# Optimization experiments

Hardware: AMD Instinct MI355X
Metric: run time of the kernel (lower is better)

Reference implementation:

```python
import jax, jax.numpy as jnp
import numpy as np

EPS = 1e-6

def _rmsnorm(x, scale):
    # RMSNorm over last axis (TPNorm pre-norm)
    var = jnp.mean(jnp.square(x), axis=-1, keepdims=True)
    return x * jax.lax.rsqrt(var + EPS) * scale


def setup_inputs() -> dict:
    key = jax.random.key(0)
    ks = jax.random.split(key, 6)
    B, S, D, H, Dh = 2, 2048, 1024, 16, 64
    x = jax.random.normal(ks[0], (B, S, D), dtype=jnp.float32)
    norm_scale = jnp.ones((D,), dtype=jnp.float32)
    # lecun_normal-like scaling: std = 1/sqrt(fan_in)
    wq = jax.random.normal(ks[1], (D, H, Dh), dtype=jnp.float32) / np.sqrt(D)
    wk = jax.random.normal(ks[2], (D, H, Dh), dtype=jnp.float32) / np.sqrt(D)
    wv = jax.random.normal(ks[3], (D, H, Dh), dtype=jnp.float32) / np.sqrt(D)
    w_out = jax.random.normal(ks[4], (H, Dh, D), dtype=jnp.float32) / np.sqrt(H * Dh)
    b_out = jnp.zeros((D,), dtype=jnp.float32)
    return {"x": x, "norm_scale": norm_scale, "wq": wq, "wk": wk, "wv": wv,
            "w_out": w_out, "b_out": b_out}


def reference(x, norm_scale, wq, wk, wv, w_out, b_out):
    dtype = x.dtype
    softmax_dtype = jnp.float32
    h = _rmsnorm(x, norm_scale)                                  # [B,S,D]
    q = jnp.einsum('bsd,dhe->bshe', h, wq)                       # [B,S,H,Dh]
    k = jnp.einsum('bsd,dhe->bshe', h, wk)
    v = jnp.einsum('bsd,dhe->bshe', h, wv)
    head_dim = q.shape[-1]
    scale = head_dim ** (-0.5)
    q = (q * scale).astype(softmax_dtype)
    kf = k.astype(softmax_dtype)
    weights = jnp.einsum('bqhd,bkhd->bhqk', q, kf)               # [B,H,S,S] fp32
    weights = jax.nn.softmax(weights, axis=-1).astype(dtype)
    new_vals = jnp.einsum('bhqk,bkhd->bqhd', weights, v).astype(dtype)
    out = jnp.einsum('bqhe,hed->bqd', new_vals, w_out) + b_out   # [B,S,D]
    return out
```

## Files before the change

kernel.cpp:

```cpp
#include <hip/hip_runtime.h>

typedef unsigned short u16;
typedef unsigned int   u32;
typedef __attribute__((ext_vector_type(8))) short bf16x8;
typedef __attribute__((ext_vector_type(4))) float f32x4;

#define SEQ 2048
#define DIM 1024
#define NH  16
#define DH  64
#define NROW 4096

static __device__ __forceinline__ u16 f2bf(float f){
  u32 u; __builtin_memcpy(&u, &f, 4);
  u32 r = (u + 0x7fffu + ((u >> 16) & 1u)) >> 16;
  return (u16)r;
}
static __device__ __forceinline__ u32 pack2bf(float a, float b){
  u32 ua, ub; __builtin_memcpy(&ua, &a, 4); __builtin_memcpy(&ub, &b, 4);
  return ((ua + 0x8000u) >> 16) | ((ub + 0x8000u) & 0xFFFF0000u);
}
static __device__ __forceinline__ u32 cvt_pk_bf16(float a, float b){
  u32 r;
  asm("v_cvt_pk_bf16_f32 %0, %1, %2" : "=v"(r) : "v"(a), "v"(b));
  return r;
}

#define GLD_LDS(gp, lp) \
  __builtin_amdgcn_global_load_lds( \
      (const __attribute__((address_space(1))) void*)(gp), \
      (__attribute__((address_space(3))) void*)(lp), 16, 0, 0)

#define WAIT_VM(N) asm volatile("s_waitcnt vmcnt(" #N ")" ::: "memory")
#define CFENCE()   asm volatile("" ::: "memory")

__global__ __launch_bounds__(256) void k_rmsnorm(const float* __restrict__ x,
                                                 const float* __restrict__ sc,
                                                 u16* __restrict__ h){
  int row = blockIdx.x, t = threadIdx.x;
  float4 v = ((const float4*)(x + (size_t)row * DIM))[t];
  float ss = v.x*v.x + v.y*v.y + v.z*v.z + v.w*v.w;
  #pragma unroll
  for (int d = 32; d; d >>= 1) ss += __shfl_down(ss, d, 64);
  __shared__ float red[4];
  if ((t & 63) == 0) red[t >> 6] = ss;
  __syncthreads();
  float tot = red[0] + red[1] + red[2] + red[3];
  float rms = rsqrtf(tot * (1.0f / DIM) + 1e-6f);
  float4 s4 = ((const float4*)sc)[t];
  u16 ov[4];
  ov[0] = f2bf(v.x * rms * s4.x);
  ov[1] = f2bf(v.y * rms * s4.y);
  ov[2] = f2bf(v.z * rms * s4.z);
  ov[3] = f2bf(v.w * rms * s4.w);
  ((uint2*)(h + (size_t)row * DIM))[t] = *(uint2*)ov;
}

__global__ __launch_bounds__(256) void k_wtrans(const float* __restrict__ in0,
                                                const float* __restrict__ in1,
                                                const float* __restrict__ in2,
                                                u16* __restrict__ outT){
  __shared__ u16 tile[64][68];
  int t = threadIdx.x;
  int c0 = blockIdx.x * 64;
  int r0 = blockIdx.y * 64;
  int z = blockIdx.z;
  const float* in = (z == 0) ? in0 : ((z == 1) ? in1 : in2);
  u16* out = outT + (size_t)z * (1u << 20);
  #pragma unroll
  for (int i = 0; i < 4; i++){
    int idx = t + 256 * i;
    int r = idx >> 4, c4 = (idx & 15) * 4;
    float4 v = *(const float4*)&in[(size_t)(r0 + r) * 1024 + c0 + c4];
    u16 pk[4] = {f2bf(v.x), f2bf(v.y), f2bf(v.z), f2bf(v.w)};
    *(uint2*)&tile[r][c4] = *(uint2*)pk;
  }
  __syncthreads();
  #pragma unroll
  for (int i = 0; i < 2; i++){
    int c = t + 256 * i;
    int n = c >> 3, koff = (c & 7) * 8;
    alignas(16) u16 vals[8];
    #pragma unroll
    for (int j = 0; j < 8; j++) vals[j] = tile[koff + j][n];
    *(uint4*)&out[(size_t)(c0 + n) * 1024 + r0 + koff] = *(uint4*)vals;
  }
}

__global__ __launch_bounds__(256) void k_gemm(const u16* __restrict__ A,
                                              const u16* __restrict__ B0,
                                              const u16* __restrict__ B1,
                                              const u16* __restrict__ B2,
                                              void* __restrict__ C0,
                                              void* __restrict__ C1,
                                              void* __restrict__ C2,
                                              const float* __restrict__ bias,
                                              int qkv){
  __shared__ u16 Al[3][128][32];
  __shared__ u16 Bl[3][128][32];
  int t = threadIdx.x, lane = t & 63, w = t >> 6;
  int wm = w & 1, wn = w >> 1;
  int mrow = lane & 15, quad = lane >> 4;

  int nwgs = qkv ? 768 : 256;
  int cpx = nwgs >> 3;
  int id = blockIdx.x;
  int wg = (id & 7) * cpx + (id >> 3);
  int z = wg >> 8;
  int rem = wg & 255;
  int m0 = (rem >> 3) << 7;
  int n0 = (rem & 7) << 7;
  const u16* Bt = (z == 0) ? B0 : ((z == 1) ? B1 : B2);

  int r0s = (t * 16) >> 6, off0 = ((t * 16) & 63) >> 1;
  int r1s = r0s + 64;

  const u16* Ap0 = &A [(size_t)(m0 + r0s) * 1024 + off0];
  const u16* Ap1 = &A [(size_t)(m0 + r1s) * 1024 + off0];
  const u16* Bp0 = &Bt[(size_t)(n0 + r0s) * 1024 + off0];
  const u16* Bp1 = &Bt[(size_t)(n0 + r1s) * 1024 + off0];

  f32x4 acc[4][4];
  #pragma unroll
  for (int ms = 0; ms < 4; ms++)
    #pragma unroll
    for (int ns = 0; ns < 4; ns++) acc[ms][ns] = (f32x4){0.f, 0.f, 0.f, 0.f};

  GLD_LDS(Ap0,      &Al[0][r0s][off0]);
  GLD_LDS(Ap1,      &Al[0][r1s][off0]);
  GLD_LDS(Bp0,      &Bl[0][r0s][off0]);
  GLD_LDS(Bp1,      &Bl[0][r1s][off0]);
  GLD_LDS(Ap0 + 32, &Al[1][r0s][off0]);
  GLD_LDS(Ap1 + 32, &Al[1][r1s][off0]);
  GLD_LDS(Bp0 + 32, &Bl[1][r0s][off0]);
  GLD_LDS(Bp1 + 32, &Bl[1][r1s][off0]);

  int cur = 0, pf = 2;
  for (int kt = 0; kt < 32; kt++){
    if (kt < 31) WAIT_VM(4); else WAIT_VM(0);
    __builtin_amdgcn_s_barrier();
    CFENCE();
    if (kt < 30){
      int K2 = (kt + 2) * 32;
      GLD_LDS(Ap0 + K2, &Al[pf][r0s][off0]);
      GLD_LDS(Ap1 + K2, &Al[pf][r1s][off0]);
      GLD_LDS(Bp0 + K2, &Bl[pf][r0s][off0]);
      GLD_LDS(Bp1 + K2, &Bl[pf][r1s][off0]);
    }
    bf16x8 af[4], bfr[4];
    #pragma unroll
    for (int ms = 0; ms < 4; ms++)
      af[ms] = *(const bf16x8*)&Al[cur][wm * 64 + ms * 16 + mrow][quad * 8];
    #pragma unroll
    for (int ns = 0; ns < 4; ns++)
      bfr[ns] = *(const bf16x8*)&Bl[cur][wn * 64 + ns * 16 + mrow][quad * 8];
    #pragma unroll
    for (int ms = 0; ms < 4; ms++)
      #pragma unroll
      for (int ns = 0; ns < 4; ns++)
        acc[ms][ns] = __builtin_amdgcn_mfma_f32_16x16x32_bf16(af[ms], bfr[ns], acc[ms][ns], 0, 0, 0);
    cur = (cur == 2) ? 0 : cur + 1;
    pf  = (pf  == 2) ? 0 : pf  + 1;
  }

  float qscale = (qkv && z == 0) ? 0.180336880111112f : 1.0f;
  bool  vmode  = (qkv && z == 2);
  void* C = (z == 0) ? C0 : ((z == 1) ? C1 : C2);

  #pragma unroll
  for (int ms = 0; ms < 4; ms++){
    #pragma unroll
    for (int ns = 0; ns < 4; ns++){
      int col = n0 + wn * 64 + ns * 16 + mrow;
      int rbase = m0 + wm * 64 + ms * 16 + quad * 4;
      if (vmode){
        int b = rbase >> 11, sl = rbase & 2047;
        int hh = col >> 6, e = col & 63;
        uint2 pk = { pack2bf(acc[ms][ns][0], acc[ms][ns][1]),
                     pack2bf(acc[ms][ns][2], acc[ms][ns][3]) };
        *(uint2*)&((u16*)C)[(size_t)((b * NH + hh) * DH + e) * SEQ + sl] = pk;
      } else if (qkv){
        #pragma unroll
        for (int r = 0; r < 4; r++)
          ((u16*)C)[(size_t)(rbase + r) * 1024 + col] = f2bf(acc[ms][ns][r] * qscale);
      } else {
        float bv = bias ? bias[col] : 0.f;
        #pragma unroll
        for (int r = 0; r < 4; r++)
          ((float*)C)[(size_t)(rbase + r) * 1024 + col] = acc[ms][ns][r] + bv;
      }
    }
  }
}

__global__ __launch_bounds__(256) void k_attn(const u16* q,
                                              const u16* __restrict__ k,
                                              const u16* __restrict__ vt,
                                              u16* nv){
  __shared__ u16 Kl[3][64][64];
  __shared__ u16 Vl[3][64][64];
  int t = threadIdx.x, lane = t & 63, w = t >> 6;
  int mrow = lane & 15, quad = lane >> 4;
  int id = blockIdx.x;
  int wg = (id & 7) * 64 + (id >> 3);
  int s0 = (wg & 15) * 128;
  int bh = wg >> 4; int b = bh >> 4, hh = bh & 15;

  const u16* qrow0 = q + (size_t)((b * SEQ + s0 + w * 32 + mrow) * NH + hh) * DH;
  const u16* qrow1 = qrow0 + 16 * NH * DH;
  bf16x8 bq[2][2];
  bq[0][0] = *(const bf16x8*)(qrow0 + quad * 8);
  bq[0][1] = *(const bf16x8*)(qrow0 + 32 + quad * 8);
  bq[1][0] = *(const bf16x8*)(qrow1 + quad * 8);
  bq[1][1] = *(const bf16x8*)(qrow1 + 32 + quad * 8);

  int rw  = t >> 3;
  int fst = (rw & 3) | (((t >> 6) & 1) << 2);
  int lc  = (t & 7) ^ fst;
  const u16* kp = k  + ((size_t)b * SEQ + rw) * (NH * DH) + hh * DH + lc * 8;
  const u16* vp = vt + ((size_t)bh * DH + rw) * SEQ + lc * 8;

  int row0 = ((mrow >> 2) << 3) | (mrow & 3);
  int cK = (quad ^ ((mrow & 3) | (((mrow >> 2) & 1) << 2))) << 4;
  int cV = (quad ^ ((mrow & 3) | (((mrow >> 3) & 1) << 2))) << 4;

  f32x4 o[2][4];
  #pragma unroll
  for (int qg = 0; qg < 2; qg++)
    #pragma unroll
    for (int g = 0; g < 4; g++) o[qg][g] = (f32x4){0.f, 0.f, 0.f, 0.f};
  f32x4 accl[2];
  accl[0] = (f32x4){0.f, 0.f, 0.f, 0.f};
  accl[1] = (f32x4){0.f, 0.f, 0.f, 0.f};
  bf16x8 onesf;
  #pragma unroll
  for (int j = 0; j < 8; j++) onesf[j] = (short)0x3F80;

  #pragma unroll
  for (int pt = 0; pt < 2; pt++){
    u16* dK = (u16*)Kl[pt]; u16* dV = (u16*)Vl[pt];
    GLD_LDS(kp,                dK + (t << 3));
    GLD_LDS(kp + 32 * NH * DH, dK + 2048 + (t << 3));
    GLD_LDS(vp,                dV + (t << 3));
    GLD_LDS(vp + 32 * SEQ,     dV + 2048 + (t << 3));
    kp += 64 * NH * DH; vp += 64;
  }

  int cur = 0, pf = 2;
  for (int kt = 0; kt < 32; kt++){
    if (kt < 31) WAIT_VM(4); else WAIT_VM(0);
    __builtin_amdgcn_s_barrier();
    CFENCE();
    if (kt < 30){
      u16* dK = (u16*)Kl[pf]; u16* dV = (u16*)Vl[pf];
      GLD_LDS(kp,                dK + (t << 3));
      GLD_LDS(kp + 32 * NH * DH, dK + 2048 + (t << 3));
      GLD_LDS(vp,                dV + (t << 3));
      GLD_LDS(vp + 32 * SEQ,     dV + 2048 + (t << 3));
      kp += 64 * NH * DH; vp += 64;
    }

    const char* Kb = (const char*)Kl[cur];
    f32x4 sT[2][4];
    __builtin_amdgcn_s_setprio(1);
    #pragma unroll
    for (int g = 0; g < 4; g++){
      int rg = row0 + ((g & 1) << 2) + ((g >> 1) << 5);
      const char* rp = Kb + rg * 128;
      bf16x8 a0 = *(const bf16x8*)(rp + cK);
      bf16x8 a1 = *(const bf16x8*)(rp + (cK ^ 64));
      f32x4 z0 = (f32x4){0.f, 0.f, 0.f, 0.f};
      f32x4 z1 = (f32x4){0.f, 0.f, 0.f, 0.f};
      z0 = __builtin_amdgcn_mfma_f32_16x16x32_bf16(a0, bq[0][0], z0, 0, 0, 0);
      z1 = __builtin_amdgcn_mfma_f32_16x16x32_bf16(a0, bq[1][0], z1, 0, 0, 0);
      z0 = __builtin_amdgcn_mfma_f32_16x16x32_bf16(a1, bq[0][1], z0, 0, 0, 0);
      z1 = __builtin_amdgcn_mfma_f32_16x16x32_bf16(a1, bq[1][1], z1, 0, 0, 0);
      sT[0][g] = z0; sT[1][g] = z1;
    }
    __builtin_amdgcn_s_setprio(0);

    bf16x8 pb[2][2];
    #pragma unroll
    for (int qg = 0; qg < 2; qg++){
      u32 wd[8];
      #pragma unroll
      for (int g = 0; g < 4; g++){
        float e0 = __builtin_amdgcn_exp2f(sT[qg][g][0]);
        float e1 = __builtin_amdgcn_exp2f(sT[qg][g][1]);
        float e2 = __builtin_amdgcn_exp2f(sT[qg][g][2]);
        float e3 = __builtin_amdgcn_exp2f(sT[qg][g][3]);
        wd[g * 2]     = cvt_pk_bf16(e0, e1);
        wd[g * 2 + 1] = cvt_pk_bf16(e2, e3);
      }
      union { u32 u[4]; bf16x8 v; } U0, U1;
      U0.u[0] = wd[0]; U0.u[1] = wd[1]; U0.u[2] = wd[2]; U0.u[3] = wd[3];
      U1.u[0] = wd[4]; U1.u[1] = wd[5]; U1.u[2] = wd[6]; U1.u[3] = wd[7];
      pb[qg][0] = U0.v; pb[qg][1] = U1.v;
    }

    __builtin_amdgcn_s_setprio(1);
    #pragma unroll
    for (int qg = 0; qg < 2; qg++){
      accl[qg] = __builtin_amdgcn_mfma_f32_16x16x32_bf16(onesf, pb[qg][0], accl[qg], 0, 0, 0);
      accl[qg] = __builtin_amdgcn_mfma_f32_16x16x32_bf16(onesf, pb[qg][1], accl[qg], 0, 0, 0);
    }

    const char* Vb = (const char*)Vl[cur];
    #pragma unroll
    for (int ge = 0; ge < 4; ge++){
      const char* rp = Vb + (ge * 16 + mrow) * 128;
      bf16x8 v0 = *(const bf16x8*)(rp + cV);
      bf16x8 v1 = *(const bf16x8*)(rp + (cV ^ 64));
      o[0][ge] = __builtin_amdgcn_mfma_f32_16x16x32_bf16(v0, pb[0][0], o[0][ge], 0, 0, 0);
      o[1][ge] = __builtin_amdgcn_mfma_f32_16x16x32_bf16(v0, pb[1][0], o[1][ge], 0, 0, 0);
      o[0][ge] = __builtin_amdgcn_mfma_f32_16x16x32_bf16(v1, pb[0][1], o[0][ge], 0, 0, 0);
      o[1][ge] = __builtin_amdgcn_mfma_f32_16x16x32_bf16(v1, pb[1][1], o[1][ge], 0, 0, 0);
    }
    __builtin_amdgcn_s_setprio(0);

    cur = (cur == 2) ? 0 : cur + 1;
    pf  = (pf  == 2) ? 0 : pf  + 1;
  }

  float rl0 = 1.0f / accl[0][0];
  float rl1 = 1.0f / accl[1][0];
  u16* orow0 = nv + (size_t)((b * SEQ + s0 + w * 32 + mrow) * NH + hh) * DH;
  u16* orow1 = orow0 + 16 * NH * DH;
  #pragma unroll
  for (int ge = 0; ge < 4; ge++){
    uint2 pk0 = { cvt_pk_bf16(o[0][ge][0] * rl0, o[0][ge][1] * rl0),
                  cvt_pk_bf16(o[0][ge][2] * rl0, o[0][ge][3] * rl0) };
    *(uint2*)&orow0[ge * 16 + quad * 4] = pk0;
    uint2 pk1 = { cvt_pk_bf16(o[1][ge][0] * rl1, o[1][ge][1] * rl1),
                  cvt_pk_bf16(o[1][ge][2] * rl1, o[1][ge][3] * rl1) };
    *(uint2*)&orow1[ge * 16 + quad * 4] = pk1;
  }
}

extern "C" void kernel_launch(void* const* d_in, const int* in_sizes, int n_in,
                              void* d_out, int out_size, void* d_ws, size_t ws_size,
                              hipStream_t stream){
  const float* x   = (const float*)d_in[0];
  const float* nsc = (const float*)d_in[1];
  const float* wq  = (const float*)d_in[2];
  const float* wk  = (const float*)d_in[3];
  const float* wv  = (const float*)d_in[4];
  const float* wo  = (const float*)d_in[5];
  const float* bo  = (const float*)d_in[6];
  char* ws = (char*)d_ws;
  const size_t MB = (size_t)1 << 20;

  u16* qb  = (u16*)(ws);
  u16* kb  = (u16*)(ws + 8  * MB);
  u16* vtb = (u16*)(ws + 16 * MB);
  u16* h   = (u16*)d_out;
  u16* wT  = (u16*)((char*)d_out + 8 * MB);
  u16* wqT = wT;
  u16* wkT = wT + (1u << 20);
  u16* wvT = wT + (2u << 20);
  u16* woT = kb;

  k_rmsnorm<<<NROW, 256, 0, stream>>>(x, nsc, h);
  k_wtrans<<<dim3(16, 16, 3), 256, 0, stream>>>(wq, wk, wv, wT);
  k_gemm<<<dim3(768), 256, 0, stream>>>(h, wqT, wkT, wvT, qb, kb, vtb, nullptr, 1);
  k_attn<<<dim3(512), 256, 0, stream>>>(qb, kb, vtb, qb);
  k_wtrans<<<dim3(16, 16, 1), 256, 0, stream>>>(wo, wo, wo, woT);
  k_gemm<<<dim3(256), 256, 0, stream>>>(qb, woT, woT, woT, d_out, d_out, d_out, bo, 0);
}
```

Before: 206.8 us.

## Halve attention KV tile to 32 keys and raise occupancy hint

The attention kernel now streams keys and values in 32-row tiles instead of 64, running twice as many loop iterations with half the LDS per stage. The LDS swizzle for the V tile is redesigned for the new 32-column layout, and launch bounds request 6 blocks per SIMD. The aim is to cut LDS and register footprint so more waves stay resident and hide latency. In exchange there are twice as many barriers and loop-overhead iterations, less MFMA work per barrier, and a risk of register spills under the tighter bound.

New measurement: 251.5 us. +21.6%, slower.

```diff
diff --git a/kernel.cpp b/kernel.cpp
--- a/kernel.cpp
+++ b/kernel.cpp
@@ -193,12 +193,12 @@
   }
 }
 
-__global__ __launch_bounds__(256) void k_attn(const u16* q,
-                                              const u16* __restrict__ k,
-                                              const u16* __restrict__ vt,
-                                              u16* nv){
-  __shared__ u16 Kl[3][64][64];
-  __shared__ u16 Vl[3][64][64];
+__global__ __launch_bounds__(256, 6) void k_attn(const u16* q,
+                                                 const u16* __restrict__ k,
+                                                 const u16* __restrict__ vt,
+                                                 u16* nv){
+  __shared__ u16 Kl[3][32][64];
+  __shared__ u16 Vl[3][32][64];
   int t = threadIdx.x, lane = t & 63, w = t >> 6;
   int mrow = lane & 15, quad = lane >> 4;
   int id = blockIdx.x;
@@ -214,15 +214,22 @@
   bq[1][0] = *(const bf16x8*)(qrow1 + quad * 8);
   bq[1][1] = *(const bf16x8*)(qrow1 + 32 + quad * 8);
 
-  int rw  = t >> 3;
-  int fst = (rw & 3) | (((t >> 6) & 1) << 2);
-  int lc  = (t & 7) ^ fst;
-  const u16* kp = k  + ((size_t)b * SEQ + rw) * (NH * DH) + hh * DH + lc * 8;
-  const u16* vp = vt + ((size_t)bh * DH + rw) * SEQ + lc * 8;
+  int rK  = t >> 3;
+  int fK  = (rK & 3) | (((rK >> 3) & 1) << 2);
+  int lcK = (t & 7) ^ fK;
+  const u16* kp = k + ((size_t)b * SEQ + rK) * (NH * DH) + hh * DH + lcK * 8;
+
+  int rV  = t >> 3;
+  int fV  = (rV & 3) | (((rV >> 2) & 1) << 2);
+  int clV = (t & 7) ^ fV;
+  int eV  = 2 * rV + (clV >> 2);
+  const u16* vp = vt + ((size_t)bh * DH + eV) * SEQ + (clV & 3) * 8;
 
   int row0 = ((mrow >> 2) << 3) | (mrow & 3);
-  int cK = (quad ^ ((mrow & 3) | (((mrow >> 2) & 1) << 2))) << 4;
-  int cV = (quad ^ ((mrow & 3) | (((mrow >> 3) & 1) << 2))) << 4;
+  int cKb = (quad ^ ((mrow & 3) | (((mrow >> 2) & 1) << 2))) << 4;
+  int cVb = ((quad ^ ((mrow >> 1) & 3)) |
+             (((mrow ^ (mrow >> 3)) & 1) << 2)) << 4;
+  int vro = (mrow >> 1) * 128;
 
   f32x4 o[2][4];
   #pragma unroll
@@ -238,37 +245,30 @@
 
   #pragma unroll
   for (int pt = 0; pt < 2; pt++){
-    u16* dK = (u16*)Kl[pt]; u16* dV = (u16*)Vl[pt];
-    GLD_LDS(kp,                dK + (t << 3));
-    GLD_LDS(kp + 32 * NH * DH, dK + 2048 + (t << 3));
-    GLD_LDS(vp,                dV + (t << 3));
-    GLD_LDS(vp + 32 * SEQ,     dV + 2048 + (t << 3));
-    kp += 64 * NH * DH; vp += 64;
+    GLD_LDS(kp, (u16*)Kl[pt] + (t << 3));
+    GLD_LDS(vp, (u16*)Vl[pt] + (t << 3));
+    kp += 32 * NH * DH; vp += 32;
   }
 
   int cur = 0, pf = 2;
-  for (int kt = 0; kt < 32; kt++){
-    if (kt < 31) WAIT_VM(4); else WAIT_VM(0);
+  for (int kt = 0; kt < 64; kt++){
+    if (kt < 63) WAIT_VM(2); else WAIT_VM(0);
     __builtin_amdgcn_s_barrier();
     CFENCE();
-    if (kt < 30){
-      u16* dK = (u16*)Kl[pf]; u16* dV = (u16*)Vl[pf];
-      GLD_LDS(kp,                dK + (t << 3));
-      GLD_LDS(kp + 32 * NH * DH, dK + 2048 + (t << 3));
-      GLD_LDS(vp,                dV + (t << 3));
-      GLD_LDS(vp + 32 * SEQ,     dV + 2048 + (t << 3));
-      kp += 64 * NH * DH; vp += 64;
+    if (kt < 62){
+      GLD_LDS(kp, (u16*)Kl[pf] + (t << 3));
+      GLD_LDS(vp, (u16*)Vl[pf] + (t << 3));
+      kp += 32 * NH * DH; vp += 32;
     }
 
     const char* Kb = (const char*)Kl[cur];
-    f32x4 sT[2][4];
+    f32x4 sT[2][2];
     __builtin_amdgcn_s_setprio(1);
     #pragma unroll
-    for (int g = 0; g < 4; g++){
-      int rg = row0 + ((g & 1) << 2) + ((g >> 1) << 5);
-      const char* rp = Kb + rg * 128;
-      bf16x8 a0 = *(const bf16x8*)(rp + cK);
-      bf16x8 a1 = *(const bf16x8*)(rp + (cK ^ 64));
+    for (int g = 0; g < 2; g++){
+      const char* rp = Kb + (row0 + (g << 2)) * 128;
+      bf16x8 a0 = *(const bf16x8*)(rp + cKb);
+      bf16x8 a1 = *(const bf16x8*)(rp + (cKb ^ 64));
       f32x4 z0 = (f32x4){0.f, 0.f, 0.f, 0.f};
       f32x4 z1 = (f32x4){0.f, 0.f, 0.f, 0.f};
       z0 = __builtin_amdgcn_mfma_f32_16x16x32_bf16(a0, bq[0][0], z0, 0, 0, 0);
@@ -279,12 +279,12 @@
     }
     __builtin_amdgcn_s_setprio(0);
 
-    bf16x8 pb[2][2];
+    bf16x8 pb[2];
     #pragma unroll
     for (int qg = 0; qg < 2; qg++){
-      u32 wd[8];
+      u32 wd[4];
       #pragma unroll
-      for (int g = 0; g < 4; g++){
+      for (int g = 0; g < 2; g++){
         float e0 = __builtin_amdgcn_exp2f(sT[qg][g][0]);
         float e1 = __builtin_amdgcn_exp2f(sT[qg][g][1]);
         float e2 = __builtin_amdgcn_exp2f(sT[qg][g][2]);
@@ -292,29 +292,21 @@
         wd[g * 2]     = cvt_pk_bf16(e0, e1);
         wd[g * 2 + 1] = cvt_pk_bf16(e2, e3);
       }
-      union { u32 u[4]; bf16x8 v; } U0, U1;
-      U0.u[0] = wd[0]; U0.u[1] = wd[1]; U0.u[2] = wd[2]; U0.u[3] = wd[3];
-      U1.u[0] = wd[4]; U1.u[1] = wd[5]; U1.u[2] = wd[6]; U1.u[3] = wd[7];
-      pb[qg][0] = U0.v; pb[qg][1] = U1.v;
+      union { u32 u[4]; bf16x8 v; } U;
+      U.u[0] = wd[0]; U.u[1] = wd[1]; U.u[2] = wd[2]; U.u[3] = wd[3];
+      pb[qg] = U.v;
     }
 
     __builtin_amdgcn_s_setprio(1);
-    #pragma unroll
-    for (int qg = 0; qg < 2; qg++){
-      accl[qg] = __builtin_amdgcn_mfma_f32_16x16x32_bf16(onesf, pb[qg][0], accl[qg], 0, 0, 0);
-      accl[qg] = __builtin_amdgcn_mfma_f32_16x16x32_bf16(onesf, pb[qg][1], accl[qg], 0, 0, 0);
-    }
+    accl[0] = __builtin_amdgcn_mfma_f32_16x16x32_bf16(onesf, pb[0], accl[0], 0, 0, 0);
+    accl[1] = __builtin_amdgcn_mfma_f32_16x16x32_bf16(onesf, pb[1], accl[1], 0, 0, 0);
 
     const char* Vb = (const char*)Vl[cur];
     #pragma unroll
     for (int ge = 0; ge < 4; ge++){
-      const char* rp = Vb + (ge * 16 + mrow) * 128;
-      bf16x8 v0 = *(const bf16x8*)(rp + cV);
-      bf16x8 v1 = *(const bf16x8*)(rp + (cV ^ 64));
-      o[0][ge] = __builtin_amdgcn_mfma_f32_16x16x32_bf16(v0, pb[0][0], o[0][ge], 0, 0, 0);
-      o[1][ge] = __builtin_amdgcn_mfma_f32_16x16x32_bf16(v0, pb[1][0], o[1][ge], 0, 0, 0);
-      o[0][ge] = __builtin_amdgcn_mfma_f32_16x16x32_bf16(v1, pb[0][1], o[0][ge], 0, 0, 0);
-      o[1][ge] = __builtin_amdgcn_mfma_f32_16x16x32_bf16(v1, pb[1][1], o[1][ge], 0, 0, 0);
+      bf16x8 vf = *(const bf16x8*)(Vb + ge * 1024 + vro + cVb);
+      o[0][ge] = __builtin_amdgcn_mfma_f32_16x16x32_bf16(vf, pb[0], o[0][ge], 0, 0, 0);
+      o[1][ge] = __builtin_amdgcn_mfma_f32_16x16x32_bf16(vf, pb[1], o[1][ge], 0, 0, 0);
     }
     __builtin_amdgcn_s_setprio(0);
 
```
